# Kernel tuning notes

Hardware: AMD Instinct MI355X
Metric: run time of the kernel (lower is better)

## Reference

```python
import jax, jax.numpy as jnp
import numpy as np

N_NODES = 50000
N_EDGES = 1600000
IN_F, H_F, N_C = 128, 128, 16
NEG_SLOPE = 0.2  # DGL GATConv default


def setup_inputs() -> dict:
    key = jax.random.key(0)
    ks = jax.random.split(key, 12)
    def w(k, shape, fan_in):
        return jax.random.normal(k, shape, jnp.float32) / np.float32(np.sqrt(fan_in))
    return {
        "feat": jax.random.normal(ks[0], (N_NODES, IN_F), jnp.float32),
        "src": jax.random.randint(ks[1], (N_EDGES,), 0, N_NODES, dtype=jnp.int32),
        "dst": jax.random.randint(ks[2], (N_EDGES,), 0, N_NODES, dtype=jnp.int32),
        "W1": w(ks[3], (IN_F, H_F), IN_F), "al1": w(ks[4], (H_F,), H_F), "ar1": w(ks[5], (H_F,), H_F), "b1": jnp.zeros((H_F,), jnp.float32),
        "W2": w(ks[6], (H_F, H_F), H_F), "al2": w(ks[7], (H_F,), H_F), "ar2": w(ks[8], (H_F,), H_F), "b2": jnp.zeros((H_F,), jnp.float32),
        "W3": w(ks[9], (H_F, N_C), H_F), "al3": w(ks[10], (N_C,), N_C), "ar3": w(ks[11], (N_C,), N_C), "b3": jnp.zeros((N_C,), jnp.float32),
    }


def _gat_layer(h, src, dst, W, al, ar, b):
    # DGL GATConv (1 head): ft = W h; e_ij = LeakyReLU(a_l.ft_src + a_r.ft_dst);
    # alpha = edge_softmax over incoming edges of dst; out = sum alpha * ft_src + bias
    ft = h @ W                                   # [N, out]
    el = ft @ al                                 # [N]
    er = ft @ ar                                 # [N]
    e = jax.nn.leaky_relu(el[src] + er[dst], negative_slope=NEG_SLOPE)  # [E]
    emax = jax.ops.segment_max(e, dst, num_segments=N_NODES)
    emax = jnp.where(jnp.isfinite(emax), emax, 0.0)  # guard isolated nodes
    ex = jnp.exp(e - emax[dst])                  # [E]
    esum = jax.ops.segment_sum(ex, dst, num_segments=N_NODES)  # [N]
    agg = jax.ops.segment_sum(ex[:, None] * ft[src], dst, num_segments=N_NODES)  # [N, out]
    out = agg / jnp.where(esum > 0, esum, 1.0)[:, None] + b
    return jax.nn.relu(out)


def reference(feat, src, dst, W1, al1, ar1, b1, W2, al2, ar2, b2, W3, al3, ar3, b3):
    h = _gat_layer(feat, src, dst, W1, al1, ar1, b1)
    h = _gat_layer(h, src, dst, W2, al2, ar2, b2)
    h = _gat_layer(h, src, dst, W3, al3, ar3, b3)
    return h  # [N_NODES, N_C]
```

## Files before the change

kernel.cpp:

```cpp
#include <hip/hip_runtime.h>
#include <hip/hip_bf16.h>

#define NN 50000
#define NE 1600000
#define FF 128
#define CC 16
#define NB ((NN + 63) / 64)
#define NBLK 256
#define CH ((NE + NBLK - 1) / NBLK)

using bf16 = __hip_bfloat16;
using bf16x8 = __attribute__((ext_vector_type(8))) short;
using f32x4  = __attribute__((ext_vector_type(4))) float;

static __device__ __forceinline__ float ldf(const void* p, int i, int isbf){
    return isbf ? __bfloat162float(((const bf16*)p)[i]) : ((const float*)p)[i];
}
static __device__ __forceinline__ float bflo(unsigned u){
    union{unsigned x; float f;} c; c.x = u << 16; return c.f;
}
static __device__ __forceinline__ float bfhi(unsigned u){
    union{unsigned x; float f;} c; c.x = u & 0xFFFF0000u; return c.f;
}
static __device__ __forceinline__ float rdlanef(float v, int l){
    return __int_as_float(__builtin_amdgcn_readlane(__float_as_int(v), l));
}
static __device__ __forceinline__ unsigned short f2bfu(float v){
    bf16 b = __float2bfloat16(v);
    union{bf16 b; unsigned short u;} c; c.b = b; return c.u;
}

__global__ __launch_bounds__(256) void k_prepcount(const unsigned short* __restrict__ featu,
                                                   const void* __restrict__ W1, const void* __restrict__ W2,
                                                   const void* __restrict__ W3, const int* __restrict__ dst,
                                                   int* __restrict__ dflag, int* __restrict__ bh,
                                                   unsigned short* __restrict__ wtg){
    __shared__ int cnt;
    __shared__ int hist[NB];
    const int t = threadIdx.x, b = blockIdx.x;
    if (t == 0) cnt = 0;
    for (int i = t; i < NB; i += 256) hist[i] = 0;
    __syncthreads();
    unsigned short lo = featu[2 * t];
    int e = (lo >> 7) & 0xFF;
    if (e >= 117 && e <= 137) atomicAdd(&cnt, 1);
    __syncthreads();
    const int isbf = (cnt >= 128) ? 1 : 0;
    int idx = b * 256 + t;
    if (idx == 0) *dflag = isbf;
    if (idx < 32768){
        int l = idx >> 14;
        int e2 = idx & 16383;
        int f = e2 >> 7, k = e2 & 127;
        const void* W = l ? W2 : W1;
        wtg[idx] = f2bfu(ldf(W, k * FF + f, isbf));
    } else if (idx < 34816){
        int e2 = idx - 32768;
        int f = e2 >> 7, k = e2 & 127;
        wtg[idx] = f2bfu(ldf(W3, k * CC + f, isbf));
    }
    const int beg = b * CH, end = (beg + CH < NE) ? beg + CH : NE;
    for (int i = beg + t; i < end; i += 256){
        int d = dst[i];
        if ((unsigned)d >= NN) d = 0;
        atomicAdd(&hist[d >> 6], 1);
    }
    __syncthreads();
    for (int k = t; k < NB; k += 256) bh[k * NBLK + b] = hist[k];
}

__global__ __launch_bounds__(256) void k_bscan(const int* __restrict__ bh, int* __restrict__ bbase,
                                               int* __restrict__ rowptr){
    __shared__ int s[256];
    const int t = threadIdx.x;
    constexpr int PT = (NB + 255) / 256;
    int loc[PT];
    int sum = 0;
    #pragma unroll
    for (int i = 0; i < PT; i++){
        int idx = t * PT + i;
        int v = 0;
        if (idx < NB){
            const int4* q = (const int4*)(bh + idx * NBLK);
            for (int j = 0; j < NBLK / 4; j++){
                int4 x = q[j];
                v += x.x + x.y + x.z + x.w;
            }
        }
        loc[i] = sum;
        sum += v;
    }
    s[t] = sum; __syncthreads();
    for (int off = 1; off < 256; off <<= 1){
        int x = (t >= off) ? s[t - off] : 0;
        __syncthreads();
        s[t] += x;
        __syncthreads();
    }
    int base = (t > 0) ? s[t - 1] : 0;
    #pragma unroll
    for (int i = 0; i < PT; i++){
        int idx = t * PT + i;
        if (idx < NB) bbase[idx] = base + loc[i];
    }
    if (t == 255){
        bbase[NB] = s[255];
        rowptr[NN] = s[255];
    }
}

__global__ __launch_bounds__(256) void k_boffset(const int* __restrict__ bbase, int* __restrict__ bh){
    int k = blockIdx.x * 4 + (threadIdx.x >> 6);
    int lane = threadIdx.x & 63;
    if (k >= NB) return;
    int v[4];
    int s = 0;
    #pragma unroll
    for (int i = 0; i < 4; i++){
        v[i] = bh[k * NBLK + 4 * lane + i];
        s += v[i];
    }
    int tot = s;
    #pragma unroll
    for (int off = 1; off < 64; off <<= 1){
        int x = __shfl_up(s, off);
        if (lane >= off) s += x;
    }
    int run = bbase[k] + s - tot;
    #pragma unroll
    for (int i = 0; i < 4; i++){
        bh[k * NBLK + 4 * lane + i] = run;
        run += v[i];
    }
}


__global__ __launch_bounds__(256) void k_fat(const int* __restrict__ src, const int* __restrict__ dst,
                                             const int* __restrict__ bh, unsigned* __restrict__ bpairs,
                                             const void* __restrict__ X, const unsigned short* __restrict__ wtg,
                                             const void* __restrict__ al, const void* __restrict__ ar,
                                             const int* __restrict__ dflag, bf16* __restrict__ ft,
                                             float* __restrict__ el, float* __restrict__ er){
    if (blockIdx.x < NBLK){
        __shared__ int cur[NB];
        const int t = threadIdx.x, b = blockIdx.x;
        for (int k = t; k < NB; k += 256) cur[k] = bh[k * NBLK + b];
        __syncthreads();
        const int beg = b * CH, end = (beg + CH < NE) ? beg + CH : NE;
        for (int i = beg + t; i < end; i += 256){
            int s = src[i];
            int d = dst[i];
            if ((unsigned)s >= NN) s = 0;
            if ((unsigned)d >= NN) d = 0;
            int p = atomicAdd(&cur[d >> 6], 1);
            if ((unsigned)p < NE) bpairs[p] = (unsigned)s | ((unsigned)(d & 63) << 16);
        }
        return;
    }
    const int isbf = *dflag;
    const int t  = threadIdx.x;
    const int n0 = (blockIdx.x - NBLK) * 64;
    const int wv = t >> 6;
    const int lane = t & 63;
    const int quad = lane >> 4;
    const int mcol = lane & 15;
    const int row = n0 + wv * 16 + mcol;
    const int rc  = (row < NN) ? row : 0;

    bf16x8 afr[4];
    if (!isbf){
        const float* xr = (const float*)X + rc * FF + quad * 8;
        #pragma unroll
        for (int kt = 0; kt < 4; kt++){
            float4 a = *(const float4*)(xr + kt * 32);
            float4 b = *(const float4*)(xr + kt * 32 + 4);
            union { bf16x8 v; unsigned u[4]; } c;
            c.u[0] = (unsigned)f2bfu(a.x) | ((unsigned)f2bfu(a.y) << 16);
            c.u[1] = (unsigned)f2bfu(a.z) | ((unsigned)f2bfu(a.w) << 16);
            c.u[2] = (unsigned)f2bfu(b.x) | ((unsigned)f2bfu(b.y) << 16);
            c.u[3] = (unsigned)f2bfu(b.z) | ((unsigned)f2bfu(b.w) << 16);
            afr[kt] = c.v;
        }
    } else {
        const unsigned short* xr = (const unsigned short*)X + rc * FF + quad * 8;
        #pragma unroll
        for (int kt = 0; kt < 4; kt++)
            afr[kt] = *(const bf16x8*)(xr + kt * 32);
    }

    float elp[4] = {0.f,0.f,0.f,0.f}, erp[4] = {0.f,0.f,0.f,0.f};

    #pragma unroll
    for (int f = 0; f < 8; f++){
        f32x4 acc = {0.f, 0.f, 0.f, 0.f};
        const unsigned short* wr = wtg + (f * 16 + mcol) * FF + quad * 8;
        #pragma unroll
        for (int kt = 0; kt < 4; kt++){
            bf16x8 bfr = *(const bf16x8*)(wr + kt * 32);
            acc = __builtin_amdgcn_mfma_f32_16x16x32_bf16(afr[kt], bfr, acc, 0, 0, 0);
        }
        int col = f * 16 + mcol;
        float alv = ldf(al, col, isbf);
        float arv = ldf(ar, col, isbf);
        #pragma unroll
        for (int reg = 0; reg < 4; reg++){
            int node = n0 + wv * 16 + quad * 4 + reg;
            float v = acc[reg];
            if (node < NN) ft[node * FF + col] = __float2bfloat16(v);
            elp[reg] += v * alv;
            erp[reg] += v * arv;
        }
    }

    #pragma unroll
    for (int reg = 0; reg < 4; reg++){
        float pl = elp[reg], pr = erp[reg];
        #pragma unroll
        for (int off = 1; off < 16; off <<= 1){
            pl += __shfl_xor(pl, off);
            pr += __shfl_xor(pr, off);
        }
        int node = n0 + wv * 16 + quad * 4 + reg;
        if (mcol == 0 && node < NN){ el[node] = pl; er[node] = pr; }
    }
}

__global__ __launch_bounds__(256) void k_bsort(const unsigned* __restrict__ bpairs, const int* __restrict__ bbase,
                                               int* __restrict__ rowptr, int* __restrict__ csrsrc){
    __shared__ int cnt[64];
    __shared__ int cur[64];
    const int t = threadIdx.x;
    const int b = blockIdx.x;
    const int base = bbase[b];
    const int endb = bbase[b + 1];
    if (t < 64) cnt[t] = 0;
    __syncthreads();
    for (int i = base + t; i < endb; i += 256)
        atomicAdd(&cnt[bpairs[i] >> 16], 1);
    __syncthreads();
    if (t < 64){
        int v = cnt[t];
        int inc = v;
        #pragma unroll
        for (int off = 1; off < 64; off <<= 1){
            int x = __shfl_up(inc, off);
            if (t >= off) inc += x;
        }
        int excl = inc - v;
        cur[t] = excl;
        int d = b * 64 + t;
        if (d < NN) rowptr[d] = base + excl;
    }
    __syncthreads();
    for (int i = base + t; i < endb; i += 256){
        unsigned pr = bpairs[i];
        int p = atomicAdd(&cur[pr >> 16], 1);
        csrsrc[base + p] = (int)(pr & 0xFFFFu);
    }
}


__global__ __launch_bounds__(256) void k_mgemm2(const void* __restrict__ X, const unsigned short* __restrict__ wtg,
                                                const void* __restrict__ al, const void* __restrict__ ar,
                                                const int* __restrict__ dflag, bf16* __restrict__ ft,
                                                float* __restrict__ el, float* __restrict__ er){
    const int isbf = *dflag;
    const int t  = threadIdx.x;
    const int n0 = blockIdx.x * 64;
    const int wv = t >> 6;
    const int lane = t & 63;
    const int quad = lane >> 4;
    const int mcol = lane & 15;
    const int row = n0 + wv * 16 + mcol;
    const int rc  = (row < NN) ? row : 0;

    bf16x8 afr[4];
    const unsigned short* xr = (const unsigned short*)X + rc * FF + quad * 8;
    #pragma unroll
    for (int kt = 0; kt < 4; kt++)
        afr[kt] = *(const bf16x8*)(xr + kt * 32);

    float elp[4] = {0.f,0.f,0.f,0.f}, erp[4] = {0.f,0.f,0.f,0.f};

    #pragma unroll
    for (int f = 0; f < 8; f++){
        f32x4 acc = {0.f, 0.f, 0.f, 0.f};
        const unsigned short* wr = wtg + (f * 16 + mcol) * FF + quad * 8;
        #pragma unroll
        for (int kt = 0; kt < 4; kt++){
            bf16x8 bfr = *(const bf16x8*)(wr + kt * 32);
            acc = __builtin_amdgcn_mfma_f32_16x16x32_bf16(afr[kt], bfr, acc, 0, 0, 0);
        }
        int col = f * 16 + mcol;
        float alv = ldf(al, col, isbf);
        float arv = ldf(ar, col, isbf);
        #pragma unroll
        for (int reg = 0; reg < 4; reg++){
            int node = n0 + wv * 16 + quad * 4 + reg;
            float v = acc[reg];
            if (node < NN) ft[node * FF + col] = __float2bfloat16(v);
            elp[reg] += v * alv;
            erp[reg] += v * arv;
        }
    }

    #pragma unroll
    for (int reg = 0; reg < 4; reg++){
        float pl = elp[reg], pr = erp[reg];
        #pragma unroll
        for (int off = 1; off < 16; off <<= 1){
            pl += __shfl_xor(pl, off);
            pr += __shfl_xor(pr, off);
        }
        int node = n0 + wv * 16 + quad * 4 + reg;
        if (mcol == 0 && node < NN){ el[node] = pl; er[node] = pr; }
    }
}


__global__ __launch_bounds__(256) void k_mgemm3(const void* __restrict__ X, const unsigned short* __restrict__ wt3g,
                                                const void* __restrict__ al, const void* __restrict__ ar,
                                                const int* __restrict__ dflag, float* __restrict__ ft,
                                                float* __restrict__ el, float* __restrict__ er){
    const int isbf = *dflag;
    const int t  = threadIdx.x;
    const int n0 = blockIdx.x * 64;
    const int wv = t >> 6;
    const int lane = t & 63;
    const int quad = lane >> 4;
    const int mcol = lane & 15;
    const int row = n0 + wv * 16 + mcol;
    const int rc  = (row < NN) ? row : 0;

    const unsigned short* xr = (const unsigned short*)X + rc * FF + quad * 8;
    const unsigned short* wr = wt3g + mcol * FF + quad * 8;

    f32x4 acc = {0.f, 0.f, 0.f, 0.f};
    #pragma unroll
    for (int kt = 0; kt < 4; kt++){
        bf16x8 afr = *(const bf16x8*)(xr + kt * 32);
        bf16x8 bfr = *(const bf16x8*)(wr + kt * 32);
        acc = __builtin_amdgcn_mfma_f32_16x16x32_bf16(afr, bfr, acc, 0, 0, 0);
    }

    float alv = ldf(al, mcol, isbf);
    float arv = ldf(ar, mcol, isbf);
    #pragma unroll
    for (int reg = 0; reg < 4; reg++){
        int node = n0 + wv * 16 + quad * 4 + reg;
        float v = acc[reg];
        if (node < NN) ft[node * CC + mcol] = v;
        float pl = v * alv, pr = v * arv;
        #pragma unroll
        for (int off = 1; off < 16; off <<= 1){
            pl += __shfl_xor(pl, off);
            pr += __shfl_xor(pr, off);
        }
        if (mcol == 0 && node < NN){ el[node] = pl; er[node] = pr; }
    }
}


__global__ __launch_bounds__(256) void k_agg128(const void* __restrict__ ftv, const float* __restrict__ el,
                                                const float* __restrict__ er, const int* __restrict__ rowptr,
                                                const int* __restrict__ csrsrc, const void* __restrict__ bias,
                                                const int* __restrict__ dflag, unsigned* __restrict__ outp){
    const int isbf = *dflag;
    int lane = threadIdx.x & 63;
    int n = blockIdx.x * 4 + (threadIdx.x >> 6);
    if (n >= NN) return;
    int beg = rowptr[n], end = rowptr[n + 1];
    beg = (beg < 0) ? 0 : (beg > NE ? NE : beg);
    end = (end < beg) ? beg : (end > NE ? NE : end);
    int deg = end - beg;
    float erd = er[n];

    float m = -3.4e38f;
    int   s_c = 0;
    float e_c = 0.f;
    for (int i = beg + lane; i < end; i += 64){
        int s = csrsrc[i];
        if ((unsigned)s >= NN) s = 0;
        float e = el[s] + erd;
        e = (e >= 0.f) ? e : 0.2f * e;
        if (i < beg + 64){ s_c = s; e_c = e; }
        m = fmaxf(m, e);
    }
    #pragma unroll
    for (int off = 32; off; off >>= 1) m = fmaxf(m, __shfl_xor(m, off));

    int jmax = (deg < 64) ? deg : 64;
    float w_c = (lane < jmax) ? __expf(e_c - m) : 0.f;
    float lsum = w_c;
    #pragma unroll
    for (int off = 32; off; off >>= 1) lsum += __shfl_xor(lsum, off);

    const unsigned* ftb = (const unsigned*)ftv;
    float acc0 = 0.f, acc1 = 0.f;
    int j = 0;
    if (jmax >= 8){
        float w[8]; unsigned u[8];
        #pragma unroll
        for (int q = 0; q < 8; q++){
            int s = __builtin_amdgcn_readlane(s_c, q);
            w[q] = rdlanef(w_c, q);
            u[q] = (ftb + s * 64)[lane];
        }
        for (j = 8; j + 8 <= jmax; j += 8){
            float wn[8]; unsigned un[8];
            #pragma unroll
            for (int q = 0; q < 8; q++){
                int s = __builtin_amdgcn_readlane(s_c, j + q);
                wn[q] = rdlanef(w_c, j + q);
                un[q] = (ftb + s * 64)[lane];
            }
            #pragma unroll
            for (int q = 0; q < 8; q++){
                acc0 += w[q] * bflo(u[q]);
                acc1 += w[q] * bfhi(u[q]);
                w[q] = wn[q]; u[q] = un[q];
            }
        }
        #pragma unroll
        for (int q = 0; q < 8; q++){
            acc0 += w[q] * bflo(u[q]);
            acc1 += w[q] * bfhi(u[q]);
        }
    }
    for (; j < jmax; ++j){
        int s = __builtin_amdgcn_readlane(s_c, j);
        float w = rdlanef(w_c, j);
        unsigned u = (ftb + s * 64)[lane];
        acc0 += w * bflo(u); acc1 += w * bfhi(u);
    }
    for (int i = beg + 64; i < end; ++i){
        int s = csrsrc[i];
        if ((unsigned)s >= NN) s = 0;
        float e = el[s] + erd;
        e = (e >= 0.f) ? e : 0.2f * e;
        float w = __expf(e - m);
        unsigned u = (ftb + s * 64)[lane];
        lsum += w;
        acc0 += w * bflo(u); acc1 += w * bfhi(u);
    }
    float inv = 1.f / ((lsum > 0.f) ? lsum : 1.f);
    float o0 = fmaxf(acc0 * inv + ldf(bias, 2 * lane,     isbf), 0.f);
    float o1 = fmaxf(acc1 * inv + ldf(bias, 2 * lane + 1, isbf), 0.f);
    unsigned pk = (unsigned)f2bfu(o0) | ((unsigned)f2bfu(o1) << 16);
    outp[n * 64 + lane] = pk;
}


__global__ __launch_bounds__(256) void k_agg16(const float* __restrict__ ftv, const float* __restrict__ el,
                                               const float* __restrict__ er, const int* __restrict__ rowptr,
                                               const int* __restrict__ csrsrc, const void* __restrict__ bias,
                                               const int* __restrict__ dflag, void* __restrict__ outp){
    const int isbf = *dflag;
    const int lane = threadIdx.x & 63;
    const int n = blockIdx.x * 4 + (threadIdx.x >> 6);
    if (n >= NN) return;
    int beg = rowptr[n], end = rowptr[n + 1];
    beg = (beg < 0) ? 0 : (beg > NE ? NE : beg);
    end = (end < beg) ? beg : (end > NE ? NE : end);
    const float erd = er[n];

    const int g = lane >> 2;
    const int c = lane & 3;
    const float4* ftq = (const float4*)ftv;
    float a0 = 0.f, a1 = 0.f, a2 = 0.f, a3 = 0.f;
    float lsum = 0.f;

    for (int j = beg; j < end; j += 32){
        #pragma unroll
        for (int q = 0; q < 2; q++){
            int iq = j + q * 16 + g;
            int cq = (iq < end) ? iq : beg;
            int s  = csrsrc[cq];
            if ((unsigned)s >= NN) s = 0;
            float e = el[s] + erd;
            e = (e >= 0.f) ? e : 0.2f * e;
            float w = (iq < end) ? __expf(e) : 0.f;
            float4 u = ftq[(unsigned)s * 4u + c];
            lsum += w;
            a0 += w * u.x; a1 += w * u.y; a2 += w * u.z; a3 += w * u.w;
        }
    }

    #pragma unroll
    for (int off = 4; off < 64; off <<= 1){
        a0 += __shfl_xor(a0, off);
        a1 += __shfl_xor(a1, off);
        a2 += __shfl_xor(a2, off);
        a3 += __shfl_xor(a3, off);
        lsum += __shfl_xor(lsum, off);
    }

    if (lane < 4){
        float inv = (lsum > 0.f) ? 1.f / lsum : 0.f;
        float o0 = fmaxf(a0 * inv + ldf(bias, c * 4 + 0, isbf), 0.f);
        float o1 = fmaxf(a1 * inv + ldf(bias, c * 4 + 1, isbf), 0.f);
        float o2 = fmaxf(a2 * inv + ldf(bias, c * 4 + 2, isbf), 0.f);
        float o3 = fmaxf(a3 * inv + ldf(bias, c * 4 + 3, isbf), 0.f);
        if (isbf){
            uint2 pk;
            pk.x = (unsigned)f2bfu(o0) | ((unsigned)f2bfu(o1) << 16);
            pk.y = (unsigned)f2bfu(o2) | ((unsigned)f2bfu(o3) << 16);
            ((uint2*)outp)[n * 4 + c] = pk;
        } else {
            float4 o; o.x = o0; o.y = o1; o.z = o2; o.w = o3;
            ((float4*)outp)[n * 4 + c] = o;
        }
    }
}


static size_t align256(size_t x){ return (x + 255) & ~(size_t)255; }

extern "C" void kernel_launch(void* const* d_in, const int* in_sizes, int n_in,
                              void* d_out, int out_size, void* d_ws, size_t ws_size,
                              hipStream_t stream) {
    const void* feat = d_in[0];
    const int*  src  = (const int*)d_in[1];
    const int*  dst  = (const int*)d_in[2];
    const void* W1 = d_in[3];
    const void* al1= d_in[4];
    const void* ar1= d_in[5];
    const void* b1 = d_in[6];
    const void* W2 = d_in[7];
    const void* al2= d_in[8];
    const void* ar2= d_in[9];
    const void* b2 = d_in[10];
    const void* W3 = d_in[11];
    const void* al3= d_in[12];
    const void* ar3= d_in[13];
    const void* b3 = d_in[14];

    char* p = (char*)d_ws;
    size_t off = 0;
    auto carve = [&](size_t bytes)->void*{
        void* r = p + off;
        off += align256(bytes);
        return r;
    };
    float* ftA   = (float*)carve((size_t)NN * FF * 4);
    unsigned* hB = (unsigned*)carve((size_t)NN * FF * 4);
    float* el    = (float*)carve((size_t)NN * 4);
    float* er    = (float*)carve((size_t)NN * 4);
    int*   rowptr= (int*)  carve((size_t)(NN + 1) * 4);
    int*   csrsrc= (int*)  carve((size_t)NE * 4);
    int*   bbase  =(int*)  carve((size_t)(NB + 1) * 4);
    int*   bh     =(int*)  carve((size_t)NB * NBLK * 4);
    unsigned short* wtg = (unsigned short*)carve((size_t)34816 * 2);
    int*   dflag  =(int*)  carve(256);
    unsigned* bpairs = (unsigned*)hB;
    void*  ftb   = ftA;
    (void)ws_size; (void)n_in; (void)in_sizes; (void)out_size;

    dim3 b256(256);
    const int mg_grid   = (NN + 63) / 64;
    const int node_grid = (NN + 3) / 4;

    k_prepcount<<<dim3(NBLK), b256, 0, stream>>>((const unsigned short*)feat, W1, W2, W3, dst, dflag, bh, wtg);
    k_bscan<<<dim3(1), b256, 0, stream>>>(bh, bbase, rowptr);
    k_boffset<<<dim3((NB + 3) / 4), b256, 0, stream>>>(bbase, bh);
    k_fat<<<dim3(NBLK + mg_grid), b256, 0, stream>>>(src, dst, bh, bpairs, feat, wtg, al1, ar1,
                                                     dflag, (bf16*)ftb, el, er);
    k_bsort<<<dim3(NB), b256, 0, stream>>>(bpairs, bbase, rowptr, csrsrc);

    k_agg128<<<dim3(node_grid), b256, 0, stream>>>(ftb, el, er, rowptr, csrsrc, b1, dflag, hB);
    k_mgemm2<<<dim3(mg_grid), b256, 0, stream>>>(hB, wtg + 16384, al2, ar2, dflag, (bf16*)ftb, el, er);
    k_agg128<<<dim3(node_grid), b256, 0, stream>>>(ftb, el, er, rowptr, csrsrc, b2, dflag, hB);
    k_mgemm3<<<dim3(mg_grid), b256, 0, stream>>>(hB, wtg + 32768, al3, ar3, dflag, (float*)ftb, el, er);
    k_agg16<<<dim3(node_grid), b256, 0, stream>>>((const float*)ftb, el, er, rowptr, csrsrc, b3, dflag, d_out);
}
```

Baseline: 345.4 us.

## Sort CSR sources by source tile and precompute bucket totals via atomics

The per-bucket edge totals are now accumulated with global atomics in the histogram kernel, so the single-block scan no longer has to read the whole NB×NBLK histogram. The bucket sort also sub-keys each destination's edges by the high bits of the source index (8 source tiles), so each CSR row lists its sources grouped by region. This is meant to improve cache locality of the feature gathers in the aggregation kernels. The cost is a memset, extra global atomics, and a larger shared-memory scan in the sort kernel.

Result: faster. 332.3 us (-3.8%).

```diff
diff --git a/kernel.cpp b/kernel.cpp
--- a/kernel.cpp
+++ b/kernel.cpp
@@ -8,6 +8,8 @@
 #define NB ((NN + 63) / 64)
 #define NBLK 256
 #define CH ((NE + NBLK - 1) / NBLK)
+#define TSH 13
+#define NT 8
 
 using bf16 = __hip_bfloat16;
 using bf16x8 = __attribute__((ext_vector_type(8))) short;
@@ -34,7 +36,7 @@
                                                    const void* __restrict__ W1, const void* __restrict__ W2,
                                                    const void* __restrict__ W3, const int* __restrict__ dst,
                                                    int* __restrict__ dflag, int* __restrict__ bh,
-                                                   unsigned short* __restrict__ wtg){
+                                                   int* __restrict__ bcounts, unsigned short* __restrict__ wtg){
     __shared__ int cnt;
     __shared__ int hist[NB];
     const int t = threadIdx.x, b = blockIdx.x;
@@ -66,10 +68,14 @@
         atomicAdd(&hist[d >> 6], 1);
     }
     __syncthreads();
-    for (int k = t; k < NB; k += 256) bh[k * NBLK + b] = hist[k];
-}
-
-__global__ __launch_bounds__(256) void k_bscan(const int* __restrict__ bh, int* __restrict__ bbase,
+    for (int k = t; k < NB; k += 256){
+        int v = hist[k];
+        bh[k * NBLK + b] = v;
+        if (v) atomicAdd(&bcounts[k], v);
+    }
+}
+
+__global__ __launch_bounds__(256) void k_bscan(const int* __restrict__ bcounts, int* __restrict__ bbase,
                                                int* __restrict__ rowptr){
     __shared__ int s[256];
     const int t = threadIdx.x;
@@ -79,14 +85,7 @@
     #pragma unroll
     for (int i = 0; i < PT; i++){
         int idx = t * PT + i;
-        int v = 0;
-        if (idx < NB){
-            const int4* q = (const int4*)(bh + idx * NBLK);
-            for (int j = 0; j < NBLK / 4; j++){
-                int4 x = q[j];
-                v += x.x + x.y + x.z + x.w;
-            }
-        }
+        int v = (idx < NB) ? bcounts[idx] : 0;
         loc[i] = sum;
         sum += v;
     }
@@ -225,36 +224,45 @@
     }
 }
 
+
 __global__ __launch_bounds__(256) void k_bsort(const unsigned* __restrict__ bpairs, const int* __restrict__ bbase,
                                                int* __restrict__ rowptr, int* __restrict__ csrsrc){
-    __shared__ int cnt[64];
-    __shared__ int cur[64];
+    __shared__ int cnt[512];
+    __shared__ int cur[512];
+    __shared__ int s[256];
     const int t = threadIdx.x;
     const int b = blockIdx.x;
     const int base = bbase[b];
     const int endb = bbase[b + 1];
-    if (t < 64) cnt[t] = 0;
-    __syncthreads();
-    for (int i = base + t; i < endb; i += 256)
-        atomicAdd(&cnt[bpairs[i] >> 16], 1);
-    __syncthreads();
-    if (t < 64){
-        int v = cnt[t];
-        int inc = v;
-        #pragma unroll
-        for (int off = 1; off < 64; off <<= 1){
-            int x = __shfl_up(inc, off);
-            if (t >= off) inc += x;
-        }
-        int excl = inc - v;
-        cur[t] = excl;
-        int d = b * 64 + t;
-        if (d < NN) rowptr[d] = base + excl;
-    }
+    cnt[2 * t] = 0; cnt[2 * t + 1] = 0;
     __syncthreads();
     for (int i = base + t; i < endb; i += 256){
         unsigned pr = bpairs[i];
-        int p = atomicAdd(&cur[pr >> 16], 1);
+        int key = (int)((pr >> 16) << 3) | (int)((pr & 0xFFFFu) >> TSH);
+        atomicAdd(&cnt[key], 1);
+    }
+    __syncthreads();
+    int v0 = cnt[2 * t], v1 = cnt[2 * t + 1];
+    s[t] = v0 + v1;
+    __syncthreads();
+    for (int off = 1; off < 256; off <<= 1){
+        int x = (t >= off) ? s[t - off] : 0;
+        __syncthreads();
+        s[t] += x;
+        __syncthreads();
+    }
+    int excl = (t > 0) ? s[t - 1] : 0;
+    cur[2 * t] = excl;
+    cur[2 * t + 1] = excl + v0;
+    if ((t & 3) == 0){
+        int d = b * 64 + (t >> 2);
+        if (d < NN) rowptr[d] = base + excl;
+    }
+    __syncthreads();
+    for (int i = base + t; i < endb; i += 256){
+        unsigned pr = bpairs[i];
+        int key = (int)((pr >> 16) << 3) | (int)((pr & 0xFFFFu) >> TSH);
+        int p = atomicAdd(&cur[key], 1);
         csrsrc[base + p] = (int)(pr & 0xFFFFu);
     }
 }
@@ -548,6 +556,7 @@
     float* er    = (float*)carve((size_t)NN * 4);
     int*   rowptr= (int*)  carve((size_t)(NN + 1) * 4);
     int*   csrsrc= (int*)  carve((size_t)NE * 4);
+    int*   bcounts=(int*)  carve((size_t)NB * 4);
     int*   bbase  =(int*)  carve((size_t)(NB + 1) * 4);
     int*   bh     =(int*)  carve((size_t)NB * NBLK * 4);
     unsigned short* wtg = (unsigned short*)carve((size_t)34816 * 2);
@@ -560,8 +569,10 @@
     const int mg_grid   = (NN + 63) / 64;
     const int node_grid = (NN + 3) / 4;
 
-    k_prepcount<<<dim3(NBLK), b256, 0, stream>>>((const unsigned short*)feat, W1, W2, W3, dst, dflag, bh, wtg);
-    k_bscan<<<dim3(1), b256, 0, stream>>>(bh, bbase, rowptr);
+    hipMemsetAsync(bcounts, 0, (size_t)NB * 4, stream);
+    k_prepcount<<<dim3(NBLK), b256, 0, stream>>>((const unsigned short*)feat, W1, W2, W3, dst,
+                                                 dflag, bh, bcounts, wtg);
+    k_bscan<<<dim3(1), b256, 0, stream>>>(bcounts, bbase, rowptr);
     k_boffset<<<dim3((NB + 3) / 4), b256, 0, stream>>>(bbase, bh);
     k_fat<<<dim3(NBLK + mg_grid), b256, 0, stream>>>(src, dst, bh, bpairs, feat, wtg, al1, ar1,
                                                      dflag, (bf16*)ftb, el, er);
```

## Vectorize edge loads, precompute bucket totals, cache bucket pairs in LDS

Applied to the files above, without the earlier changes.

Edge-chunk processing in the count and scatter passes now reads src/dst as int4 vectors with a fixed chunk size of 6400. The count kernel also atomically accumulates per-bucket totals, so the single-block scan no longer sums the full per-block histogram matrix. The bucket sort keeps up to 4096 pairs in shared memory between its two passes to avoid a second global read. The fixed CH relies on NE being divisible by 4 and by NBLK, which holds for these sizes. The change also adds global atomics and a memset launch.

After: 322.7 us. -6.6%, faster.

```diff
diff --git a/kernel.cpp b/kernel.cpp
--- a/kernel.cpp
+++ b/kernel.cpp
@@ -7,7 +7,8 @@
 #define CC 16
 #define NB ((NN + 63) / 64)
 #define NBLK 256
-#define CH ((NE + NBLK - 1) / NBLK)
+#define CH 6400
+#define EBUF 4096
 
 using bf16 = __hip_bfloat16;
 using bf16x8 = __attribute__((ext_vector_type(8))) short;
@@ -29,12 +30,13 @@
     bf16 b = __float2bfloat16(v);
     union{bf16 b; unsigned short u;} c; c.b = b; return c.u;
 }
+static __device__ __forceinline__ int clampn(int v){ return ((unsigned)v >= NN) ? 0 : v; }
 
 __global__ __launch_bounds__(256) void k_prepcount(const unsigned short* __restrict__ featu,
                                                    const void* __restrict__ W1, const void* __restrict__ W2,
                                                    const void* __restrict__ W3, const int* __restrict__ dst,
                                                    int* __restrict__ dflag, int* __restrict__ bh,
-                                                   unsigned short* __restrict__ wtg){
+                                                   int* __restrict__ bcounts, unsigned short* __restrict__ wtg){
     __shared__ int cnt;
     __shared__ int hist[NB];
     const int t = threadIdx.x, b = blockIdx.x;
@@ -59,17 +61,28 @@
         int f = e2 >> 7, k = e2 & 127;
         wtg[idx] = f2bfu(ldf(W3, k * CC + f, isbf));
     }
-    const int beg = b * CH, end = (beg + CH < NE) ? beg + CH : NE;
-    for (int i = beg + t; i < end; i += 256){
-        int d = dst[i];
-        if ((unsigned)d >= NN) d = 0;
-        atomicAdd(&hist[d >> 6], 1);
+    const int beg = b * CH;
+    const int end = (beg + CH < NE) ? beg + CH : NE;
+    if (end > beg){
+        const int4* d4 = (const int4*)(dst + beg);
+        const int n4 = (end - beg) >> 2;
+        for (int i = t; i < n4; i += 256){
+            int4 d = d4[i];
+            atomicAdd(&hist[clampn(d.x) >> 6], 1);
+            atomicAdd(&hist[clampn(d.y) >> 6], 1);
+            atomicAdd(&hist[clampn(d.z) >> 6], 1);
+            atomicAdd(&hist[clampn(d.w) >> 6], 1);
+        }
     }
     __syncthreads();
-    for (int k = t; k < NB; k += 256) bh[k * NBLK + b] = hist[k];
-}
-
-__global__ __launch_bounds__(256) void k_bscan(const int* __restrict__ bh, int* __restrict__ bbase,
+    for (int k = t; k < NB; k += 256){
+        int v = hist[k];
+        bh[k * NBLK + b] = v;
+        if (v) atomicAdd(&bcounts[k], v);
+    }
+}
+
+__global__ __launch_bounds__(256) void k_bscan(const int* __restrict__ bcounts, int* __restrict__ bbase,
                                                int* __restrict__ rowptr){
     __shared__ int s[256];
     const int t = threadIdx.x;
@@ -79,14 +92,7 @@
     #pragma unroll
     for (int i = 0; i < PT; i++){
         int idx = t * PT + i;
-        int v = 0;
-        if (idx < NB){
-            const int4* q = (const int4*)(bh + idx * NBLK);
-            for (int j = 0; j < NBLK / 4; j++){
-                int4 x = q[j];
-                v += x.x + x.y + x.z + x.w;
-            }
-        }
+        int v = (idx < NB) ? bcounts[idx] : 0;
         loc[i] = sum;
         sum += v;
     }
@@ -146,14 +152,29 @@
         const int t = threadIdx.x, b = blockIdx.x;
         for (int k = t; k < NB; k += 256) cur[k] = bh[k * NBLK + b];
         __syncthreads();
-        const int beg = b * CH, end = (beg + CH < NE) ? beg + CH : NE;
-        for (int i = beg + t; i < end; i += 256){
-            int s = src[i];
-            int d = dst[i];
-            if ((unsigned)s >= NN) s = 0;
-            if ((unsigned)d >= NN) d = 0;
-            int p = atomicAdd(&cur[d >> 6], 1);
-            if ((unsigned)p < NE) bpairs[p] = (unsigned)s | ((unsigned)(d & 63) << 16);
+        const int beg = b * CH;
+        const int end = (beg + CH < NE) ? beg + CH : NE;
+        if (end > beg){
+            const int4* s4 = (const int4*)(src + beg);
+            const int4* d4 = (const int4*)(dst + beg);
+            const int n4 = (end - beg) >> 2;
+            for (int i = t; i < n4; i += 256){
+                int4 sv = s4[i];
+                int4 dv = d4[i];
+                int ss, dd, p;
+                ss = clampn(sv.x); dd = clampn(dv.x);
+                p = atomicAdd(&cur[dd >> 6], 1);
+                if ((unsigned)p < NE) bpairs[p] = (unsigned)ss | ((unsigned)(dd & 63) << 16);
+                ss = clampn(sv.y); dd = clampn(dv.y);
+                p = atomicAdd(&cur[dd >> 6], 1);
+                if ((unsigned)p < NE) bpairs[p] = (unsigned)ss | ((unsigned)(dd & 63) << 16);
+                ss = clampn(sv.z); dd = clampn(dv.z);
+                p = atomicAdd(&cur[dd >> 6], 1);
+                if ((unsigned)p < NE) bpairs[p] = (unsigned)ss | ((unsigned)(dd & 63) << 16);
+                ss = clampn(sv.w); dd = clampn(dv.w);
+                p = atomicAdd(&cur[dd >> 6], 1);
+                if ((unsigned)p < NE) bpairs[p] = (unsigned)ss | ((unsigned)(dd & 63) << 16);
+            }
         }
         return;
     }
@@ -225,18 +246,24 @@
     }
 }
 
+
 __global__ __launch_bounds__(256) void k_bsort(const unsigned* __restrict__ bpairs, const int* __restrict__ bbase,
                                                int* __restrict__ rowptr, int* __restrict__ csrsrc){
     __shared__ int cnt[64];
     __shared__ int cur[64];
+    __shared__ unsigned ebuf[EBUF];
     const int t = threadIdx.x;
     const int b = blockIdx.x;
     const int base = bbase[b];
     const int endb = bbase[b + 1];
     if (t < 64) cnt[t] = 0;
     __syncthreads();
-    for (int i = base + t; i < endb; i += 256)
-        atomicAdd(&cnt[bpairs[i] >> 16], 1);
+    for (int i = base + t; i < endb; i += 256){
+        unsigned pr = bpairs[i];
+        int k = i - base;
+        if (k < EBUF) ebuf[k] = pr;
+        atomicAdd(&cnt[pr >> 16], 1);
+    }
     __syncthreads();
     if (t < 64){
         int v = cnt[t];
@@ -253,7 +280,8 @@
     }
     __syncthreads();
     for (int i = base + t; i < endb; i += 256){
-        unsigned pr = bpairs[i];
+        int k = i - base;
+        unsigned pr = (k < EBUF) ? ebuf[k] : bpairs[i];
         int p = atomicAdd(&cur[pr >> 16], 1);
         csrsrc[base + p] = (int)(pr & 0xFFFFu);
     }
@@ -548,6 +576,7 @@
     float* er    = (float*)carve((size_t)NN * 4);
     int*   rowptr= (int*)  carve((size_t)(NN + 1) * 4);
     int*   csrsrc= (int*)  carve((size_t)NE * 4);
+    int*   bcounts=(int*)  carve((size_t)NB * 4);
     int*   bbase  =(int*)  carve((size_t)(NB + 1) * 4);
     int*   bh     =(int*)  carve((size_t)NB * NBLK * 4);
     unsigned short* wtg = (unsigned short*)carve((size_t)34816 * 2);
@@ -560,8 +589,10 @@
     const int mg_grid   = (NN + 63) / 64;
     const int node_grid = (NN + 3) / 4;
 
-    k_prepcount<<<dim3(NBLK), b256, 0, stream>>>((const unsigned short*)feat, W1, W2, W3, dst, dflag, bh, wtg);
-    k_bscan<<<dim3(1), b256, 0, stream>>>(bh, bbase, rowptr);
+    hipMemsetAsync(bcounts, 0, (size_t)NB * 4, stream);
+    k_prepcount<<<dim3(NBLK), b256, 0, stream>>>((const unsigned short*)feat, W1, W2, W3, dst,
+                                                 dflag, bh, bcounts, wtg);
+    k_bscan<<<dim3(1), b256, 0, stream>>>(bcounts, bbase, rowptr);
     k_boffset<<<dim3((NB + 3) / 4), b256, 0, stream>>>(bbase, bh);
     k_fat<<<dim3(NBLK + mg_grid), b256, 0, stream>>>(src, dst, bh, bpairs, feat, wtg, al1, ar1,
                                                      dflag, (bf16*)ftb, el, er);
```
